# Kernel optimization log

Hardware: AMD Instinct MI355X
Metric: run time of the kernel (lower is better)

The kernel has to match this reference:

```python
import jax, jax.numpy as jnp
import numpy as np

B, S, D, H = 4, 2048, 1024, 16
HD = D // H  # head_length = 64


def setup_inputs() -> dict:
    key = jax.random.key(0)
    ks = jax.random.split(key, 11)
    s = 1.0 / np.sqrt(D)
    return {
        "queries": jax.random.normal(ks[0], (B, S, D), jnp.float32),
        "keys": jax.random.normal(ks[1], (B, S, D), jnp.float32),
        "values": jax.random.normal(ks[2], (B, S, D), jnp.float32),
        "Wq": jax.random.normal(ks[3], (D, D), jnp.float32) * s,
        "bq": jnp.zeros((D,), jnp.float32),
        "Wk": jax.random.normal(ks[4], (D, D), jnp.float32) * s,
        "bk": jnp.zeros((D,), jnp.float32),
        "Wv": jax.random.normal(ks[5], (D, D), jnp.float32) * s,
        "bv": jnp.zeros((D,), jnp.float32),
        "Wo": jax.random.normal(ks[6], (D, D), jnp.float32) * s,
        "bo": jnp.zeros((D,), jnp.float32),
    }


def reference(queries, keys, values, Wq, bq, Wk, bk, Wv, bv, Wo, bo):
    # Linear projections (torch Linear: x @ W^T + b), split into heads -> [B, H, S, HD]
    def proj(x, W, b):
        return (x @ W.T + b).reshape(B, S, H, HD).transpose(0, 2, 1, 3)

    q = proj(queries, Wq, bq)
    k = proj(keys, Wk, bk)
    v = proj(values, Wv, bv)
    # Scaled dot-product attention, scale = 1/sqrt(head_length)
    scores = jnp.einsum("bhsd,bhtd->bhst", q, k) / jnp.sqrt(jnp.float32(HD))
    attn = jax.nn.softmax(scores, axis=-1)
    out = jnp.einsum("bhst,bhtd->bhsd", attn, v)  # [B, H, S, HD]
    out = out.transpose(0, 2, 1, 3).reshape(B, S, D)
    return out @ Wo.T + bo
```

## Files before the change

### kernel.cpp

```cpp
#include <hip/hip_runtime.h>
#include <stdint.h>
#include <stddef.h>

#define B_ 4
#define S_ 2048
#define D_ 1024
#define H_ 16
#define HD_ 64

#define QSCALE 0.18033688f

typedef __bf16 bf16;
typedef __bf16 bf16x8 __attribute__((ext_vector_type(8)));
typedef __bf16 bf16x4 __attribute__((ext_vector_type(4)));
typedef float f32x4 __attribute__((ext_vector_type(4)));
typedef float f32x16 __attribute__((ext_vector_type(16)));
typedef uint32_t u32x4 __attribute__((ext_vector_type(4)));

__device__ __forceinline__ f32x4 mfma16(bf16x8 a, bf16x8 b, f32x4 c) {
  return __builtin_amdgcn_mfma_f32_16x16x32_bf16(a, b, c, 0, 0, 0);
}
__device__ __forceinline__ f32x16 mfma32(bf16x8 a, bf16x8 b, f32x16 c) {
  return __builtin_amdgcn_mfma_f32_32x32x16_bf16(a, b, c, 0, 0, 0);
}

__device__ __forceinline__ float fexp2(float x) {
#if __has_builtin(__builtin_amdgcn_exp2f)
  return __builtin_amdgcn_exp2f(x);
#else
  return exp2f(x);
#endif
}

__device__ __forceinline__ void gload_lds16(const void* g, void* l) {
  __builtin_amdgcn_global_load_lds(
      (__attribute__((address_space(1))) uint32_t*)(uintptr_t)g,
      (__attribute__((address_space(3))) uint32_t*)l, 16, 0, 0);
}

__device__ __forceinline__ uint32_t cvt_pk(float lo, float hi) {
  uint32_t r;
  asm volatile("v_cvt_pk_bf16_f32 %0, %1, %2" : "=v"(r) : "v"(lo), "v"(hi));
  return r;
}

__device__ __forceinline__ void pl_swap(uint32_t& a, uint32_t& b) {
#if __has_builtin(__builtin_amdgcn_permlane32_swap)
  typedef int i32x2_t __attribute__((ext_vector_type(2)));
  i32x2_t r = __builtin_amdgcn_permlane32_swap((int)a, (int)b, false, false);
  a = (uint32_t)r[0];
  b = (uint32_t)r[1];
#else
  uint32_t pa_ = (uint32_t)__shfl_xor((int)a, 32);
  uint32_t pb_ = (uint32_t)__shfl_xor((int)b, 32);
  bool hi_ = (threadIdx.x & 32) != 0;
  uint32_t na = hi_ ? pb_ : a;
  uint32_t nb = hi_ ? b : pa_;
  a = na;
  b = nb;
#endif
}

__device__ __forceinline__ bf16x8 pack4(uint32_t a, uint32_t b, uint32_t c,
                                        uint32_t d) {
  u32x4 v = {a, b, c, d};
  return __builtin_bit_cast(bf16x8, v);
}

__global__ __launch_bounds__(256) void convert_w(
    const float* __restrict__ a, const float* __restrict__ b,
    const float* __restrict__ c, const float* __restrict__ d,
    bf16* __restrict__ out) {
  int i = (blockIdx.x * 256 + threadIdx.x) * 4;
  const float* srcs[4] = {a, b, c, d};
#pragma unroll
  for (int w = 0; w < 4; ++w) {
    f32x4 x = *(const f32x4*)(srcs[w] + i);
    bf16x4 v;
    v[0] = (bf16)x[0]; v[1] = (bf16)x[1]; v[2] = (bf16)x[2]; v[3] = (bf16)x[3];
    *(bf16x4*)(out + (size_t)w * (D_ * D_) + i) = v;
  }
}

__global__ __launch_bounds__(256, 2) void gemm_qkv(
    const float* __restrict__ Aq, const float* __restrict__ Ak,
    const float* __restrict__ Av, const bf16* __restrict__ Wb,
    const float* __restrict__ bq, const float* __restrict__ bk,
    const float* __restrict__ bv, bf16* __restrict__ Outb) {
  __shared__ alignas(128) char lds[32768];
  const int tid = threadIdx.x;
  const int lane = tid & 63;
  const int wave = tid >> 6;
  const int m0 = blockIdx.x * 128;
  const int n0 = blockIdx.y * 128;
  const int wr = wave >> 1, wc = wave & 1;
  const int z = blockIdx.z;
  const float* A = z == 0 ? Aq : (z == 1 ? Ak : Av);
  const float* bias = z == 0 ? bq : (z == 1 ? bk : bv);
  const bf16* W = Wb + (size_t)z * (D_ * D_);
  bf16* Out = Outb + (size_t)z * ((size_t)B_ * S_ * D_);
  const float oscale = (z == 0) ? QSCALE : 1.0f;

  f32x4 acc[4][4] = {};

  for (int kt = 0; kt < 16; ++kt) {
    const int k0 = kt * 64;
#pragma unroll
    for (int j = 0; j < 4; ++j) {
      int slot = j * 256 + tid;
      int row = slot >> 3, kb = slot & 7;
      const float* src = A + (size_t)(m0 + row) * D_ + k0 + (kb << 3);
      f32x4 x0 = *(const f32x4*)src;
      f32x4 x1 = *(const f32x4*)(src + 4);
      bf16x8 v;
      v[0] = (bf16)x0[0]; v[1] = (bf16)x0[1]; v[2] = (bf16)x0[2]; v[3] = (bf16)x0[3];
      v[4] = (bf16)x1[0]; v[5] = (bf16)x1[1]; v[6] = (bf16)x1[2]; v[7] = (bf16)x1[3];
      *(bf16x8*)(lds + row * 128 + ((kb ^ (row & 7)) << 4)) = v;
    }
#pragma unroll
    for (int j = 0; j < 4; ++j) {
      int slot = j * 256 + tid;
      int row = slot >> 3, kb = slot & 7;
      gload_lds16(W + (size_t)(n0 + row) * D_ + k0 + ((kb ^ (row & 7)) << 3),
                  lds + 16384 + j * 4096 + wave * 1024);
    }
    __syncthreads();
#pragma unroll
    for (int ks = 0; ks < 2; ++ks) {
      bf16x8 af[4], bfr[4];
#pragma unroll
      for (int f = 0; f < 4; ++f) {
        int ar = wr * 64 + f * 16 + (lane & 15);
        af[f] = *(const bf16x8*)(lds + ar * 128 +
                                 (((ks * 4 + (lane >> 4)) ^ (ar & 7)) << 4));
        int br = wc * 64 + f * 16 + (lane & 15);
        bfr[f] = *(const bf16x8*)(lds + 16384 + br * 128 +
                                  (((ks * 4 + (lane >> 4)) ^ (br & 7)) << 4));
      }
#pragma unroll
      for (int i = 0; i < 4; ++i)
#pragma unroll
        for (int j = 0; j < 4; ++j)
          acc[i][j] = mfma16(af[i], bfr[j], acc[i][j]);
    }
    __syncthreads();
  }

#pragma unroll
  for (int j = 0; j < 4; ++j) {
    const int col = n0 + wc * 64 + j * 16 + (lane & 15);
    const float bv_ = bias[col];
    const int h = col >> 6, hd = col & 63;
#pragma unroll
    for (int i = 0; i < 4; ++i) {
      const int row0 = m0 + wr * 64 + i * 16 + ((lane >> 4) << 2);
      if (z != 2) {
#pragma unroll
        for (int r = 0; r < 4; ++r) {
          int row = row0 + r;
          int b = row >> 11, s = row & (S_ - 1);
          Out[(((size_t)(b * H_ + h) * S_ + s) << 6) + hd] =
              (bf16)((acc[i][j][r] + bv_) * oscale);
        }
      } else {
        int b = row0 >> 11, s0 = row0 & (S_ - 1);
        bf16x4 pk;
#pragma unroll
        for (int r = 0; r < 4; ++r) pk[r] = (bf16)(acc[i][j][r] + bv_);
        *(bf16x4*)(Out + ((size_t)(b * H_ + h) * HD_ + hd) * S_ + s0) = pk;
      }
    }
  }
}

__global__ __launch_bounds__(256, 2) void gemm_out(
    const bf16* __restrict__ A, const bf16* __restrict__ Wb,
    const float* __restrict__ bias, float* __restrict__ Out) {
  __shared__ alignas(128) char lds[32768];
  const int tid = threadIdx.x;
  const int lane = tid & 63;
  const int wave = tid >> 6;
  const int m0 = blockIdx.x * 128;
  const int n0 = blockIdx.y * 128;
  const int wr = wave >> 1, wc = wave & 1;

  f32x4 acc[4][4] = {};

  for (int kt = 0; kt < 16; ++kt) {
    const int k0 = kt * 64;
#pragma unroll
    for (int j = 0; j < 4; ++j) {
      int slot = j * 256 + tid;
      int row = slot >> 3, kb = slot & 7;
      gload_lds16(A + (size_t)(m0 + row) * D_ + k0 + ((kb ^ (row & 7)) << 3),
                  lds + j * 4096 + wave * 1024);
    }
#pragma unroll
    for (int j = 0; j < 4; ++j) {
      int slot = j * 256 + tid;
      int row = slot >> 3, kb = slot & 7;
      gload_lds16(Wb + (size_t)(n0 + row) * D_ + k0 + ((kb ^ (row & 7)) << 3),
                  lds + 16384 + j * 4096 + wave * 1024);
    }
    __syncthreads();
#pragma unroll
    for (int ks = 0; ks < 2; ++ks) {
      bf16x8 af[4], bfr[4];
#pragma unroll
      for (int f = 0; f < 4; ++f) {
        int ar = wr * 64 + f * 16 + (lane & 15);
        af[f] = *(const bf16x8*)(lds + ar * 128 +
                                 (((ks * 4 + (lane >> 4)) ^ (ar & 7)) << 4));
        int br = wc * 64 + f * 16 + (lane & 15);
        bfr[f] = *(const bf16x8*)(lds + 16384 + br * 128 +
                                  (((ks * 4 + (lane >> 4)) ^ (br & 7)) << 4));
      }
#pragma unroll
      for (int i = 0; i < 4; ++i)
#pragma unroll
        for (int j = 0; j < 4; ++j)
          acc[i][j] = mfma16(af[i], bfr[j], acc[i][j]);
    }
    __syncthreads();
  }

#pragma unroll
  for (int j = 0; j < 4; ++j) {
    const int col = n0 + wc * 64 + j * 16 + (lane & 15);
    const float bv_ = bias[col];
#pragma unroll
    for (int i = 0; i < 4; ++i) {
      const int row0 = m0 + wr * 64 + i * 16 + ((lane >> 4) << 2);
#pragma unroll
      for (int r = 0; r < 4; ++r)
        Out[(size_t)(row0 + r) * D_ + col] = acc[i][j][r] + bv_;
    }
  }
}

__global__ __launch_bounds__(256, 2) void attn_kernel(
    const bf16* __restrict__ Qh, const bf16* __restrict__ Kh,
    const bf16* __restrict__ Vt, bf16* __restrict__ AO) {
  __shared__ alignas(128) char lds[2][16384];
  const int tid = threadIdx.x, lane = tid & 63, wave = tid >> 6;
  const int hi = lane >> 5, l31 = lane & 31;
  const int bh = blockIdx.y;
  const int q0 = blockIdx.x * 256 + wave * 64;
  const bf16* Qb = Qh + (size_t)bh * S_ * HD_;
  const bf16* Kb = Kh + (size_t)bh * S_ * HD_;
  const bf16* Vb = Vt + (size_t)bh * HD_ * S_;

  bf16x8 qf[2][4];
#pragma unroll
  for (int qg = 0; qg < 2; ++qg)
#pragma unroll
    for (int ks = 0; ks < 4; ++ks)
      qf[qg][ks] = *(const bf16x8*)(Qb + (size_t)(q0 + qg * 32 + l31) * HD_ +
                                    ks * 16 + hi * 8);

  bf16x8 onesf;
#pragma unroll
  for (int j = 0; j < 8; ++j) onesf[j] = (bf16)1.0f;

  const bf16* gs[4];
  int lo_[4], ginc[4];
#pragma unroll
  for (int j = 0; j < 4; ++j) {
    int f = j * 4 + wave;
    lo_[j] = f * 1024;
    if (f < 8) {
      gs[j] = Kb + (size_t)((f >> 2) * 32 + l31) * HD_ + (f & 3) * 16 + hi * 8;
      ginc[j] = 64 * HD_;
    } else {
      int g = f - 8;
      gs[j] = Vb + (size_t)((g & 1) * 32 + l31) * S_ + (g >> 1) * 16 + hi * 8;
      ginc[j] = 64;
    }
  }

  f32x16 oacc0[2] = {}, oacc1[2] = {};
  f32x16 dacc0 = {}, dacc1 = {};

#pragma unroll
  for (int j = 0; j < 4; ++j) {
    gload_lds16(gs[j], &lds[0][lo_[j]]);
    gs[j] += ginc[j];
  }
  __syncthreads();

  for (int t = 0; t < 32; ++t) {
    const int cur = t & 1;
    if (t < 31) {
#pragma unroll
      for (int j = 0; j < 4; ++j) {
        gload_lds16(gs[j], &lds[cur ^ 1][lo_[j]]);
        gs[j] += ginc[j];
      }
    }
    const char* kbuf = lds[cur];
    const char* vbuf = lds[cur] + 8192;
#pragma unroll
    for (int kb = 0; kb < 2; ++kb) {
      f32x16 s0 = {}, s1 = {};
      __builtin_amdgcn_s_setprio(1);
#pragma unroll
      for (int ks = 0; ks < 4; ++ks) {
        bf16x8 kf = *(const bf16x8*)(kbuf + (kb * 4 + ks) * 1024 + lane * 16);
        s0 = mfma32(kf, qf[0][ks], s0);
        s1 = mfma32(kf, qf[1][ks], s1);
      }
      __builtin_amdgcn_s_setprio(0);
      bf16x8 pa[2][2];
#pragma unroll
      for (int qg = 0; qg < 2; ++qg) {
        f32x16 s = qg ? s1 : s0;
        f32x16 e;
#pragma unroll
        for (int r = 0; r < 16; ++r) e[r] = fexp2(s[r]);
        uint32_t w0 = cvt_pk(e[0], e[1]), w1 = cvt_pk(e[2], e[3]),
                 w2 = cvt_pk(e[4], e[5]), w3 = cvt_pk(e[6], e[7]),
                 w4 = cvt_pk(e[8], e[9]), w5 = cvt_pk(e[10], e[11]),
                 w6 = cvt_pk(e[12], e[13]), w7 = cvt_pk(e[14], e[15]);
        pl_swap(w0, w2);
        pl_swap(w1, w3);
        pl_swap(w4, w6);
        pl_swap(w5, w7);
        pa[qg][0] = pack4(w0, w1, w2, w3);
        pa[qg][1] = pack4(w4, w5, w6, w7);
      }
      __builtin_amdgcn_s_setprio(1);
      dacc0 = mfma32(pa[0][0], onesf, dacc0);
      dacc0 = mfma32(pa[0][1], onesf, dacc0);
      dacc1 = mfma32(pa[1][0], onesf, dacc1);
      dacc1 = mfma32(pa[1][1], onesf, dacc1);
#pragma unroll
      for (int ht = 0; ht < 2; ++ht) {
        bf16x8 vf0 =
            *(const bf16x8*)(vbuf + ((kb * 2 + 0) * 2 + ht) * 1024 + lane * 16);
        oacc0[ht] = mfma32(pa[0][0], vf0, oacc0[ht]);
        oacc1[ht] = mfma32(pa[1][0], vf0, oacc1[ht]);
        bf16x8 vf1 =
            *(const bf16x8*)(vbuf + ((kb * 2 + 1) * 2 + ht) * 1024 + lane * 16);
        oacc0[ht] = mfma32(pa[0][1], vf1, oacc0[ht]);
        oacc1[ht] = mfma32(pa[1][1], vf1, oacc1[ht]);
      }
      __builtin_amdgcn_s_setprio(0);
    }
    __syncthreads();
  }

  const int b = bh >> 4, h = bh & 15;
#pragma unroll
  for (int qg = 0; qg < 2; ++qg) {
#pragma unroll
    for (int r = 0; r < 16; ++r) {
      float rd = 1.0f / (qg ? dacc1[r] : dacc0[r]);
      int qr = (r & 3) + 8 * (r >> 2) + 4 * hi;
      size_t base = ((size_t)(b * S_ + q0 + qg * 32 + qr)) * D_ + h * 64;
      AO[base + l31] = (bf16)((qg ? oacc1[0][r] : oacc0[0][r]) * rd);
      AO[base + 32 + l31] = (bf16)((qg ? oacc1[1][r] : oacc0[1][r]) * rd);
    }
  }
}

extern "C" void kernel_launch(void* const* d_in, const int* in_sizes, int n_in,
                              void* d_out, int out_size, void* d_ws,
                              size_t ws_size, hipStream_t stream) {
  (void)in_sizes; (void)n_in; (void)out_size; (void)ws_size;
  const float* q  = (const float*)d_in[0];
  const float* k  = (const float*)d_in[1];
  const float* v  = (const float*)d_in[2];
  const float* Wq = (const float*)d_in[3];
  const float* bq = (const float*)d_in[4];
  const float* Wk = (const float*)d_in[5];
  const float* bk = (const float*)d_in[6];
  const float* Wv = (const float*)d_in[7];
  const float* bv = (const float*)d_in[8];
  const float* Wo = (const float*)d_in[9];
  const float* bo = (const float*)d_in[10];

  bf16* ws = (bf16*)d_ws;
  const size_t WSZ = (size_t)D_ * D_;
  const size_t TSZ = (size_t)B_ * S_ * D_;
  bf16* Wqkv = ws;
  bf16* Wob = ws + 3 * WSZ;
  bf16* Qh = ws + 4 * WSZ;
  bf16* Kh = Qh + TSZ;
  bf16* Vt = Qh + 2 * TSZ;
  bf16* AO = Qh + 3 * TSZ;

  convert_w<<<dim3(1024), dim3(256), 0, stream>>>(Wq, Wk, Wv, Wo, ws);
  gemm_qkv<<<dim3(64, 8, 3), dim3(256), 0, stream>>>(q, k, v, Wqkv, bq, bk, bv,
                                                     Qh);
  attn_kernel<<<dim3(8, 64), dim3(256), 0, stream>>>(Qh, Kh, Vt, AO);
  gemm_out<<<dim3(64, 8), dim3(256), 0, stream>>>(AO, Wob, bo, (float*)d_out);
}
```

Baseline: 184.5 us.

## Pre-convert QKV inputs to bf16 and run projections as separate async-load GEMMs

Replaces the fused fp32-input QKV GEMM, which converted activations to bf16 inside the K loop through registers, with a standalone conversion kernel per input followed by a bf16 GEMM. That GEMM loads both operands with direct global-to-LDS loads, and a single templated GEMM now covers all projections. The aim is to remove the register-staged fp32 load and convert from the GEMM inner loop and to halve the A-operand bytes re-read across the N tiles. The trade-off is an extra read and write of each activation tensor, plus three serialized launches where there was one, which lowers parallelism per launch.

```diff
diff --git a/kernel.cpp b/kernel.cpp
--- a/kernel.cpp
+++ b/kernel.cpp
@@ -82,11 +82,23 @@
   }
 }
 
-__global__ __launch_bounds__(256, 2) void gemm_qkv(
-    const float* __restrict__ Aq, const float* __restrict__ Ak,
-    const float* __restrict__ Av, const bf16* __restrict__ Wb,
-    const float* __restrict__ bq, const float* __restrict__ bk,
-    const float* __restrict__ bv, bf16* __restrict__ Outb) {
+__global__ __launch_bounds__(256) void convert_in(const float* __restrict__ in,
+                                                  bf16* __restrict__ out) {
+  const int n8 = (B_ * S_ * D_) / 8;
+  for (int i = blockIdx.x * 256 + threadIdx.x; i < n8; i += gridDim.x * 256) {
+    f32x4 x0 = *(const f32x4*)(in + (size_t)i * 8);
+    f32x4 x1 = *(const f32x4*)(in + (size_t)i * 8 + 4);
+    bf16x8 v;
+    v[0] = (bf16)x0[0]; v[1] = (bf16)x0[1]; v[2] = (bf16)x0[2]; v[3] = (bf16)x0[3];
+    v[4] = (bf16)x1[0]; v[5] = (bf16)x1[1]; v[6] = (bf16)x1[2]; v[7] = (bf16)x1[3];
+    *(bf16x8*)(out + (size_t)i * 8) = v;
+  }
+}
+
+template <int MODE>
+__global__ __launch_bounds__(256, 2) void gemm_bf16(
+    const bf16* __restrict__ A, const bf16* __restrict__ Wb,
+    const float* __restrict__ bias, void* __restrict__ Out, float oscale) {
   __shared__ alignas(128) char lds[32768];
   const int tid = threadIdx.x;
   const int lane = tid & 63;
@@ -94,12 +106,6 @@
   const int m0 = blockIdx.x * 128;
   const int n0 = blockIdx.y * 128;
   const int wr = wave >> 1, wc = wave & 1;
-  const int z = blockIdx.z;
-  const float* A = z == 0 ? Aq : (z == 1 ? Ak : Av);
-  const float* bias = z == 0 ? bq : (z == 1 ? bk : bv);
-  const bf16* W = Wb + (size_t)z * (D_ * D_);
-  bf16* Out = Outb + (size_t)z * ((size_t)B_ * S_ * D_);
-  const float oscale = (z == 0) ? QSCALE : 1.0f;
 
   f32x4 acc[4][4] = {};
 
@@ -109,19 +115,14 @@
     for (int j = 0; j < 4; ++j) {
       int slot = j * 256 + tid;
       int row = slot >> 3, kb = slot & 7;
-      const float* src = A + (size_t)(m0 + row) * D_ + k0 + (kb << 3);
-      f32x4 x0 = *(const f32x4*)src;
-      f32x4 x1 = *(const f32x4*)(src + 4);
-      bf16x8 v;
-      v[0] = (bf16)x0[0]; v[1] = (bf16)x0[1]; v[2] = (bf16)x0[2]; v[3] = (bf16)x0[3];
-      v[4] = (bf16)x1[0]; v[5] = (bf16)x1[1]; v[6] = (bf16)x1[2]; v[7] = (bf16)x1[3];
-      *(bf16x8*)(lds + row * 128 + ((kb ^ (row & 7)) << 4)) = v;
+      gload_lds16(A + (size_t)(m0 + row) * D_ + k0 + ((kb ^ (row & 7)) << 3),
+                  lds + j * 4096 + wave * 1024);
     }
 #pragma unroll
     for (int j = 0; j < 4; ++j) {
       int slot = j * 256 + tid;
       int row = slot >> 3, kb = slot & 7;
-      gload_lds16(W + (size_t)(n0 + row) * D_ + k0 + ((kb ^ (row & 7)) << 3),
+      gload_lds16(Wb + (size_t)(n0 + row) * D_ + k0 + ((kb ^ (row & 7)) << 3),
                   lds + 16384 + j * 4096 + wave * 1024);
     }
     __syncthreads();
@@ -154,86 +155,28 @@
 #pragma unroll
     for (int i = 0; i < 4; ++i) {
       const int row0 = m0 + wr * 64 + i * 16 + ((lane >> 4) << 2);
-      if (z != 2) {
+      if (MODE == 2) {
+        float* O = (float*)Out;
+#pragma unroll
+        for (int r = 0; r < 4; ++r)
+          O[(size_t)(row0 + r) * D_ + col] = acc[i][j][r] + bv_;
+      } else if (MODE == 0) {
+        bf16* O = (bf16*)Out;
 #pragma unroll
         for (int r = 0; r < 4; ++r) {
           int row = row0 + r;
           int b = row >> 11, s = row & (S_ - 1);
-          Out[(((size_t)(b * H_ + h) * S_ + s) << 6) + hd] =
+          O[(((size_t)(b * H_ + h) * S_ + s) << 6) + hd] =
               (bf16)((acc[i][j][r] + bv_) * oscale);
         }
       } else {
+        bf16* O = (bf16*)Out;
         int b = row0 >> 11, s0 = row0 & (S_ - 1);
         bf16x4 pk;
 #pragma unroll
         for (int r = 0; r < 4; ++r) pk[r] = (bf16)(acc[i][j][r] + bv_);
-        *(bf16x4*)(Out + ((size_t)(b * H_ + h) * HD_ + hd) * S_ + s0) = pk;
-      }
-    }
-  }
-}
-
-__global__ __launch_bounds__(256, 2) void gemm_out(
-    const bf16* __restrict__ A, const bf16* __restrict__ Wb,
-    const float* __restrict__ bias, float* __restrict__ Out) {
-  __shared__ alignas(128) char lds[32768];
-  const int tid = threadIdx.x;
-  const int lane = tid & 63;
-  const int wave = tid >> 6;
-  const int m0 = blockIdx.x * 128;
-  const int n0 = blockIdx.y * 128;
-  const int wr = wave >> 1, wc = wave & 1;
-
-  f32x4 acc[4][4] = {};
-
-  for (int kt = 0; kt < 16; ++kt) {
-    const int k0 = kt * 64;
-#pragma unroll
-    for (int j = 0; j < 4; ++j) {
-      int slot = j * 256 + tid;
-      int row = slot >> 3, kb = slot & 7;
-      gload_lds16(A + (size_t)(m0 + row) * D_ + k0 + ((kb ^ (row & 7)) << 3),
-                  lds + j * 4096 + wave * 1024);
-    }
-#pragma unroll
-    for (int j = 0; j < 4; ++j) {
-      int slot = j * 256 + tid;
-      int row = slot >> 3, kb = slot & 7;
-      gload_lds16(Wb + (size_t)(n0 + row) * D_ + k0 + ((kb ^ (row & 7)) << 3),
-                  lds + 16384 + j * 4096 + wave * 1024);
-    }
-    __syncthreads();
-#pragma unroll
-    for (int ks = 0; ks < 2; ++ks) {
-      bf16x8 af[4], bfr[4];
-#pragma unroll
-      for (int f = 0; f < 4; ++f) {
-        int ar = wr * 64 + f * 16 + (lane & 15);
-        af[f] = *(const bf16x8*)(lds + ar * 128 +
-                                 (((ks * 4 + (lane >> 4)) ^ (ar & 7)) << 4));
-        int br = wc * 64 + f * 16 + (lane & 15);
-        bfr[f] = *(const bf16x8*)(lds + 16384 + br * 128 +
-                                  (((ks * 4 + (lane >> 4)) ^ (br & 7)) << 4));
-      }
-#pragma unroll
-      for (int i = 0; i < 4; ++i)
-#pragma unroll
-        for (int j = 0; j < 4; ++j)
-          acc[i][j] = mfma16(af[i], bfr[j], acc[i][j]);
-    }
-    __syncthreads();
-  }
-
-#pragma unroll
-  for (int j = 0; j < 4; ++j) {
-    const int col = n0 + wc * 64 + j * 16 + (lane & 15);
-    const float bv_ = bias[col];
-#pragma unroll
-    for (int i = 0; i < 4; ++i) {
-      const int row0 = m0 + wr * 64 + i * 16 + ((lane >> 4) << 2);
-#pragma unroll
-      for (int r = 0; r < 4; ++r)
-        Out[(size_t)(row0 + r) * D_ + col] = acc[i][j][r] + bv_;
+        *(bf16x4*)(O + ((size_t)(b * H_ + h) * HD_ + hd) * S_ + s0) = pk;
+      }
     }
   }
 }
@@ -382,16 +325,24 @@
   bf16* ws = (bf16*)d_ws;
   const size_t WSZ = (size_t)D_ * D_;
   const size_t TSZ = (size_t)B_ * S_ * D_;
-  bf16* Wqkv = ws;
+  bf16* Wqb = ws;
+  bf16* Wkb = ws + WSZ;
+  bf16* Wvb = ws + 2 * WSZ;
   bf16* Wob = ws + 3 * WSZ;
-  bf16* Qh = ws + 4 * WSZ;
-  bf16* Kh = Qh + TSZ;
-  bf16* Vt = Qh + 2 * TSZ;
-  bf16* AO = Qh + 3 * TSZ;
+  bf16* Abf = ws + 4 * WSZ;
+  bf16* Qh  = Abf + TSZ;
+  bf16* Kh  = Qh + TSZ;
+  bf16* Vt  = Kh + TSZ;
+  bf16* AO  = Abf;
 
   convert_w<<<dim3(1024), dim3(256), 0, stream>>>(Wq, Wk, Wv, Wo, ws);
-  gemm_qkv<<<dim3(64, 8, 3), dim3(256), 0, stream>>>(q, k, v, Wqkv, bq, bk, bv,
-                                                     Qh);
-  attn_kernel<<<dim3(8, 64), dim3(256), 0, stream>>>(Qh, Kh, Vt, AO);
-  gemm_out<<<dim3(64, 8), dim3(256), 0, stream>>>(AO, Wob, bo, (float*)d_out);
-}
+  dim3 gg(64, 8), bb(256);
+  convert_in<<<dim3(2048), bb, 0, stream>>>(q, Abf);
+  gemm_bf16<0><<<gg, bb, 0, stream>>>(Abf, Wqb, bq, Qh, QSCALE);
+  convert_in<<<dim3(2048), bb, 0, stream>>>(k, Abf);
+  gemm_bf16<0><<<gg, bb, 0, stream>>>(Abf, Wkb, bk, Kh, 1.0f);
+  convert_in<<<dim3(2048), bb, 0, stream>>>(v, Abf);
+  gemm_bf16<1><<<gg, bb, 0, stream>>>(Abf, Wvb, bv, Vt, 1.0f);
+  attn_kernel<<<dim3(8, 64), bb, 0, stream>>>(Qh, Kh, Vt, AO);
+  gemm_bf16<2><<<gg, bb, 0, stream>>>(AO, Wob, bo, d_out, 1.0f);
+}
```

New measurement: 205.6 us. +11.4%, slower.
